# Optimization experiments

Hardware: AMD Instinct MI355X
Metric: run time of the kernel (lower is better)

The kernel has to match this reference:

```python
import jax, jax.numpy as jnp
import numpy as np

B, S, D, M, HID, THETA = 8, 4096, 128, 256, 256, 4096


def _impulse_response():
    """Build discretized LTI (A,B) via ZOH and the impulse response H [M, S]."""
    Q = jnp.arange(M, dtype=jnp.float32).reshape(-1, 1)          # [M,1]
    R = (2.0 * Q + 1.0) / THETA                                   # [M,1]
    ii, jj = jnp.meshgrid(jnp.arange(M), jnp.arange(M), indexing='ij')
    # (-1)^(i-j+1): -1 when (i-j) even, +1 when odd
    sign = jnp.where((ii - jj) % 2 == 0, -1.0, 1.0)
    A = R * jnp.where(ii < jj, -1.0, sign)                        # [M,M]
    Bv = R * jnp.where(jnp.arange(M).reshape(-1, 1) % 2 == 0, 1.0, -1.0)  # [M,1]
    # zero-order-hold discretization via matrix exponential of augmented system
    aug = jnp.zeros((M + 1, M + 1), dtype=jnp.float32)
    aug = aug.at[:M, :M].set(A).at[:M, M].set(Bv[:, 0])
    expA = jax.scipy.linalg.expm(aug)
    Ad, Bd = expA[:M, :M], expA[:M, M:M + 1]
    # H[:, i] = Ad^i @ Bd
    def step(Ai, _):
        return Ad @ Ai, (Ai @ Bd)[:, 0]
    _, Hs = jax.lax.scan(step, jnp.eye(M, dtype=jnp.float32), None, length=S)
    return Hs.T  # [M, S]


def setup_inputs() -> dict:
    key = jax.random.key(0)
    k1, k2, k3 = jax.random.split(key, 3)
    x = jax.random.normal(k1, (B, S, D), dtype=jnp.float32)
    W_u = jax.random.normal(k2, (D, 1), dtype=jnp.float32) / np.sqrt(D)
    b_u = jnp.zeros((1,), dtype=jnp.float32)
    W_h = jax.random.normal(k3, (M + D, HID), dtype=jnp.float32) / np.sqrt(M + D)
    b_h = jnp.zeros((HID,), dtype=jnp.float32)
    H = _impulse_response()  # [M, S], fixed (non-trainable) impulse response
    return {"x": x, "W_u": W_u, "b_u": b_u, "W_h": W_h, "b_h": b_h, "H": H}


def reference(x, W_u, b_u, W_h, b_h, H):
    batch, seq_len, _ = x.shape
    n = 2 * seq_len
    # u_t = relu(W_u x_t)  -> [B, S, 1]
    u = jax.nn.relu(jnp.einsum('bsd,do->bso', x, W_u) + b_u)
    fft_H = jnp.fft.rfft(H, n=n, axis=-1)                 # [M, S+1]
    fft_u = jnp.fft.rfft(u[..., 0], n=n, axis=-1)         # [B, S+1]
    temp = fft_u[:, None, :] * fft_H[None, :, :]          # [B, M, S+1] complex
    m = jnp.fft.irfft(temp, n=n, axis=-1)[:, :, :seq_len]  # [B, M, S]
    m = jnp.transpose(m, (0, 2, 1))                       # [B, S, M]
    input_h = jnp.concatenate([m, x], axis=-1)            # [B, S, M+D]
    h = jax.nn.relu(jnp.einsum('bsf,fh->bsh', input_h, W_h) + b_h)
    h_n = h[:, -1, :]
    return (h, h_n)
```

## Files before the change

### kernel.cpp

```cpp
#include <hip/hip_runtime.h>

#define S_LEN 4096
#define B_SZ 8
#define HN_OFF 8388608
#define CPROWS 544

typedef __attribute__((ext_vector_type(8))) short short8;
typedef __attribute__((ext_vector_type(4))) float f32x4;

typedef const __attribute__((address_space(1))) unsigned int as1_u32;
typedef __attribute__((address_space(3))) unsigned int as3_u32;

__device__ __forceinline__ void gload16(const short* g, short* l) {
  __builtin_amdgcn_global_load_lds((as1_u32*)g, (as3_u32*)l, 16, 0, 0);
}

__device__ __forceinline__ short f2bf(float f) {
  union { float f; unsigned u; } v; v.f = f;
  unsigned r = v.u + 0x7FFFu + ((v.u >> 16) & 1u);
  return (short)(r >> 16);
}

__global__ __launch_bounds__(256) void k_prep(const float* __restrict__ x,
                                              const float* __restrict__ Wu,
                                              const float* __restrict__ bu,
                                              const float* __restrict__ H,
                                              const float* __restrict__ Wh,
                                              short* __restrict__ cp,
                                              short* __restrict__ xb,
                                              short* __restrict__ Ht,
                                              short* __restrict__ wht) {
  int bx = blockIdx.x;
  if (bx >= 8520) {
    int j = (bx - 8520) * 256 + threadIdx.x;
    if (j < 256 * 384) {
      int n = j / 384, k = j % 384;
      wht[j] = f2bf(Wh[k * 256 + n]);
    }
    return;
  }
  if (bx >= 8264) {
    __shared__ short tile[64][72];
    int bx2 = bx - 8264;
    int t0 = (bx2 >> 2) << 6, q0 = (bx2 & 3) << 6;
    int tid = threadIdx.x;
    int r = tid >> 2, c0 = (tid & 3) << 4;
    const float* src = H + (size_t)(q0 + r) * S_LEN + t0 + c0;
    #pragma unroll
    for (int v4 = 0; v4 < 4; ++v4) {
      float4 hv = *(const float4*)(src + 4 * v4);
      tile[r][c0 + 4 * v4]     = f2bf(hv.x);
      tile[r][c0 + 4 * v4 + 1] = f2bf(hv.y);
      tile[r][c0 + 4 * v4 + 2] = f2bf(hv.z);
      tile[r][c0 + 4 * v4 + 3] = f2bf(hv.w);
    }
    __syncthreads();
    int s2 = tid >> 2, qc = (tid & 3) << 4;
    short8 o0, o1;
    #pragma unroll
    for (int j2 = 0; j2 < 8; ++j2) {
      o0[j2] = tile[qc + j2][s2];
      o1[j2] = tile[qc + 8 + j2][s2];
    }
    short* dst = Ht + (size_t)(t0 + s2) * 256 + q0 + qc;
    *(short8*)dst       = o0;
    *(short8*)(dst + 8) = o1;
    return;
  }
  if (bx >= 8192) {
    int idx = (bx - 8192) * 256 + threadIdx.x;
    if (idx < 18432) {
      int j = idx & 7;
      int r = 508 + ((idx >> 3) % 36);
      int rem = (idx >> 3) / 36;
      int p = rem & 7;
      int b = rem >> 3;
      int e = 8 * r + p + j;
      if (e >= S_LEN)
        cp[((size_t)(b * 8 + p) * CPROWS + r) * 8 + j] = 0;
    }
    return;
  }
  int row = bx * 4 + (threadIdx.x >> 6);
  int l = threadIdx.x & 63;
  float2 xv = *(const float2*)(x + (size_t)row * 128 + 2 * l);
  float2 wv = *(const float2*)(Wu + 2 * l);
  float s = xv.x * wv.x + xv.y * wv.y;
  #pragma unroll
  for (int m = 32; m >= 1; m >>= 1) s += __shfl_xor(s, m, 64);
  unsigned pack = (((unsigned)f2bf(xv.y) & 0xFFFFu) << 16) | ((unsigned)f2bf(xv.x) & 0xFFFFu);
  *(unsigned*)(xb + (size_t)row * 128 + 2 * l) = pack;
  float v = s + bu[0];
  v = v > 0.0f ? v : 0.0f;
  short vb = f2bf(v);
  if (l < 8) {
    int t = row & (S_LEN - 1);
    int b = row >> 12;
    int e = (S_LEN - 1) - t;
    int p = l;
    if (e >= p) {
      int d = e - p;
      cp[((size_t)(b * 8 + p) * CPROWS + (d >> 3)) * 8 + (d & 7)] = vb;
    }
  }
}

__global__ __launch_bounds__(256) void k_g(const short* __restrict__ wht,
                                           const short* __restrict__ Ht,
                                           short* __restrict__ Gt) {
  int nt = blockIdx.x & 1, tt = blockIdx.x >> 1;
  int n0 = nt << 7, t0 = tt << 7;
  int tid = threadIdx.x;
  int lane = tid & 63, wid = tid >> 6;
  int wr = wid >> 1, wc = wid & 1;
  int lm = lane & 15, kg = lane >> 4;

  const short* Abase = wht + (size_t)(n0 + wr * 64 + lm) * 384 + 8 * kg;
  const short* Bbase = Ht  + (size_t)(t0 + wc * 64 + lm) * 256 + 8 * kg;

  f32x4 acc[4][4];
  #pragma unroll
  for (int ii = 0; ii < 4; ++ii)
    #pragma unroll
    for (int jn = 0; jn < 4; ++jn)
      acc[ii][jn] = (f32x4){0.0f, 0.0f, 0.0f, 0.0f};

  #pragma unroll
  for (int c = 0; c < 4; ++c) {
    short8 a[8], bf[8];
    #pragma unroll
    for (int mf = 0; mf < 4; ++mf)
      #pragma unroll
      for (int ks = 0; ks < 2; ++ks)
        a[mf * 2 + ks] = *(const short8*)(Abase + mf * 16 * 384 + c * 64 + ks * 32);
    #pragma unroll
    for (int nf = 0; nf < 4; ++nf)
      #pragma unroll
      for (int ks = 0; ks < 2; ++ks)
        bf[nf * 2 + ks] = *(const short8*)(Bbase + nf * 16 * 256 + c * 64 + ks * 32);
    #pragma unroll
    for (int ks = 0; ks < 2; ++ks)
      #pragma unroll
      for (int mf = 0; mf < 4; ++mf)
        #pragma unroll
        for (int nf = 0; nf < 4; ++nf)
          acc[mf][nf] = __builtin_amdgcn_mfma_f32_16x16x32_bf16(a[mf * 2 + ks], bf[nf * 2 + ks], acc[mf][nf], 0, 0, 0);
  }

  #pragma unroll
  for (int mf = 0; mf < 4; ++mf)
    #pragma unroll
    for (int nf = 0; nf < 4; ++nf)
      #pragma unroll
      for (int j = 0; j < 4; ++j) {
        int n = n0 + wr * 64 + mf * 16 + kg * 4 + j;
        int t = t0 + wc * 64 + nf * 16 + lm;
        Gt[(size_t)n * S_LEN + t] = f2bf(acc[mf][nf][j]);
      }
}

__global__ __launch_bounds__(512, 2) void k_fused(const short* __restrict__ cp,
                                                  const short* __restrict__ Gt,
                                                  const short* __restrict__ xb,
                                                  const short* __restrict__ wht,
                                                  const float* __restrict__ bh,
                                                  float* __restrict__ out) {
  __shared__ __attribute__((aligned(16))) short Bt[2][128 * 128];
  __shared__ __attribute__((aligned(16))) short Aw[2][6144];

  int i = blockIdx.x;
  int kk = i >> 4;
  int nt = i & 1;
  int b  = (i >> 1) & 7;
  int n0 = nt << 7;

  int tid = threadIdx.x;
  int lane = tid & 63, wid = tid >> 6;
  int wr = wid >> 2, wc = wid & 3;
  int lm = lane & 15, kg = lane >> 4;
  int l3 = lane >> 3, l7 = lane & 7;
  int lm7 = lm & 7;

  const short* bS0 = Gt + (size_t)(n0 + wid * 16 + kg) * S_LEN + ((lm ^ kg) << 3);
  const short* bS1 = Gt + (size_t)(n0 + wid * 16 + 4 + kg) * S_LEN + ((lm ^ (kg ^ 4)) << 3);

  int dbase = 127 - 64 * wr - lm + 8 * kg;
  int aof[10];
  #pragma unroll
  for (int v = 0; v < 10; ++v) {
    int d = dbase + 16 * v - 48;
    aof[v] = ((d & ~7) | ((d & 7) ^ ((d >> 3) & 7))) << 3;
  }

  int bof[8];
  #pragma unroll
  for (int nf = 0; nf < 2; ++nf)
    #pragma unroll
    for (int ks = 0; ks < 4; ++ks)
      bof[nf * 4 + ks] = (wc * 32 + nf * 16 + lm) * 128 + (((4 * ks + kg) ^ lm7) << 3);

  int xof[16];
  #pragma unroll
  for (int mf = 0; mf < 4; ++mf)
    #pragma unroll
    for (int ks = 0; ks < 4; ++ks)
      xof[mf * 4 + ks] = (wr * 64 + mf * 16 + lm) * 128 + (((4 * ks + kg) ^ lm7) << 3);

  const short* wxBase = wht + (size_t)(n0 + wc * 32 + lm) * 384 + 256 + 8 * kg;

  for (int ph = 0; ph < 2; ++ph) {
    int st = ph ? kk : (31 - kk);
    int s0 = st << 7;
    int asbase = 496 - 16 * st;
    const short* aSrc = cp + ((size_t)(b * 8 + (l7 ^ l3)) * CPROWS + asbase + wid * 8 + l3) * 8;
    const short* xR0 = xb + (size_t)(b * S_LEN + s0 + wid * 16 + kg) * 128 + ((lm ^ kg) << 3);
    const short* xR1 = xb + (size_t)(b * S_LEN + s0 + wid * 16 + 4 + kg) * 128 + ((lm ^ (kg ^ 4)) << 3);

    int NCt = st + 1;
    int NCp = NCt + 1;

    f32x4 acc[4][2];
    #pragma unroll
    for (int ii = 0; ii < 4; ++ii)
      #pragma unroll
      for (int jn = 0; jn < 2; ++jn)
        acc[ii][jn] = (f32x4){0.0f, 0.0f, 0.0f, 0.0f};

    auto STAGE_T = [&](int cc) {
      int slot = cc & 1;
      int coff = cc * 128;
      #pragma unroll
      for (int e = 0; e < 2; ++e) {
        gload16(bS0 + (size_t)(8 * e) * S_LEN + coff, &Bt[slot][(wid * 16 + 8 * e) * 128]);
        gload16(bS1 + (size_t)(8 * e) * S_LEN + coff, &Bt[slot][(wid * 16 + 8 * e + 4) * 128]);
      }
      if (wid < 4) gload16(aSrc + coff, &Aw[slot][wid * 512]);
    };
    auto STAGE_X = [&]() {
      int slot = NCt & 1;
      #pragma unroll
      for (int e = 0; e < 2; ++e) {
        gload16(xR0 + (size_t)(8 * e) * 128, &Bt[slot][(wid * 16 + 8 * e) * 128]);
        gload16(xR1 + (size_t)(8 * e) * 128, &Bt[slot][(wid * 16 + 8 * e + 4) * 128]);
      }
    };

    asm volatile("s_waitcnt vmcnt(0) lgkmcnt(0)\n\ts_barrier" ::: "memory");
    STAGE_T(0);

    for (int c = 0; c < NCp; ++c) {
      asm volatile("s_waitcnt vmcnt(0) lgkmcnt(0)\n\ts_barrier" ::: "memory");
      if (c + 1 < NCt) STAGE_T(c + 1);
      else if (c + 1 < NCp) STAGE_X();

      if (c < NCt) {
        const short* AwB = &Aw[c & 1][0];
        const short* BtB = &Bt[c & 1][0];
        short8 A10[10];
        #pragma unroll
        for (int v = 0; v < 10; ++v) A10[v] = *(const short8*)(AwB + aof[v]);
        short8 Bf[8];
        #pragma unroll
        for (int ii = 0; ii < 8; ++ii) Bf[ii] = *(const short8*)(BtB + bof[ii]);
        __builtin_amdgcn_s_setprio(1);
        #pragma unroll
        for (int ks = 0; ks < 4; ++ks)
          #pragma unroll
          for (int mf = 0; mf < 4; ++mf)
            #pragma unroll
            for (int nf = 0; nf < 2; ++nf)
              acc[mf][nf] = __builtin_amdgcn_mfma_f32_16x16x32_bf16(
                  A10[2 * ks - mf + 3], Bf[nf * 4 + ks], acc[mf][nf], 0, 0, 0);
        __builtin_amdgcn_s_setprio(0);
      } else {
        const short* BtB = &Bt[NCt & 1][0];
        short8 Ax[16];
        #pragma unroll
        for (int ii = 0; ii < 16; ++ii) Ax[ii] = *(const short8*)(BtB + xof[ii]);
        short8 Bx[8];
        #pragma unroll
        for (int nf = 0; nf < 2; ++nf)
          #pragma unroll
          for (int ks = 0; ks < 4; ++ks)
            Bx[nf * 4 + ks] = *(const short8*)(wxBase + (size_t)nf * 16 * 384 + 32 * ks);
        __builtin_amdgcn_s_setprio(1);
        #pragma unroll
        for (int ks = 0; ks < 4; ++ks)
          #pragma unroll
          for (int mf = 0; mf < 4; ++mf)
            #pragma unroll
            for (int nf = 0; nf < 2; ++nf)
              acc[mf][nf] = __builtin_amdgcn_mfma_f32_16x16x32_bf16(
                  Ax[mf * 4 + ks], Bx[nf * 4 + ks], acc[mf][nf], 0, 0, 0);
        __builtin_amdgcn_s_setprio(0);
      }
    }

    #pragma unroll
    for (int mf = 0; mf < 4; ++mf)
      #pragma unroll
      for (int nf = 0; nf < 2; ++nf) {
        int n = n0 + wc * 32 + nf * 16 + lm;
        float bias = bh[n];
        #pragma unroll
        for (int j2 = 0; j2 < 4; ++j2) {
          int s = s0 + wr * 64 + mf * 16 + kg * 4 + j2;
          float v = acc[mf][nf][j2] + bias;
          v = v > 0.0f ? v : 0.0f;
          out[(size_t)(b * S_LEN + s) * 256 + n] = v;
          if (s == S_LEN - 1)
            out[HN_OFF + b * 256 + n] = v;
        }
      }
  }
}

extern "C" void kernel_launch(void* const* d_in, const int* in_sizes, int n_in,
                              void* d_out, int out_size, void* d_ws, size_t ws_size,
                              hipStream_t stream) {
  const float* x  = (const float*)d_in[0];
  const float* Wu = (const float*)d_in[1];
  const float* bu = (const float*)d_in[2];
  const float* Wh = (const float*)d_in[3];
  const float* bh = (const float*)d_in[4];
  const float* H  = (const float*)d_in[5];
  float* out = (float*)d_out;

  char* ws = (char*)d_ws;
  short* cp  = (short*)(ws);
  short* wht = (short*)(ws + 557056);
  short* xb  = (short*)(ws + 753664);
  short* Ht  = (short*)(ws + 9142272);
  short* Gt  = (short*)(ws + 11239424);

  k_prep<<<8904, 256, 0, stream>>>(x, Wu, bu, H, Wh, cp, xb, Ht, wht);
  k_g   <<<64,   256, 0, stream>>>(wht, Ht, Gt);
  k_fused<<<256, 512, 0, stream>>>(cp, Gt, xb, wht, bh, out);
}
```

Measured before the change: 76.34 us.

## Triple-buffer fused Toeplitz GEMM with half-K stages and interleaved loads

Restructures the fused Toeplitz-plus-x GEMM main loop to use 64-wide K chunks with a three-slot LDS ring. Loads are issued two stages ahead and split between the two MFMA half-phases, so global-to-LDS copies overlap with compute. Shared memory per block drops, which lets launch bounds target four blocks per CU instead of two. Block index mapping is also reordered so batch varies fastest. The extra barriers per stage and the higher occupancy target may add sync overhead or register pressure.

```diff
diff --git a/kernel.cpp b/kernel.cpp
--- a/kernel.cpp
+++ b/kernel.cpp
@@ -20,6 +20,8 @@
   unsigned r = v.u + 0x7FFFu + ((v.u >> 16) & 1u);
   return (short)(r >> 16);
 }
+
+#define MFMA(d, a, bb) d = __builtin_amdgcn_mfma_f32_16x16x32_bf16(a, bb, d, 0, 0, 0)
 
 __global__ __launch_bounds__(256) void k_prep(const float* __restrict__ x,
                                               const float* __restrict__ Wu,
@@ -144,7 +146,7 @@
       for (int mf = 0; mf < 4; ++mf)
         #pragma unroll
         for (int nf = 0; nf < 4; ++nf)
-          acc[mf][nf] = __builtin_amdgcn_mfma_f32_16x16x32_bf16(a[mf * 2 + ks], bf[nf * 2 + ks], acc[mf][nf], 0, 0, 0);
+          MFMA(acc[mf][nf], a[mf * 2 + ks], bf[nf * 2 + ks]);
   }
 
   #pragma unroll
@@ -159,65 +161,65 @@
       }
 }
 
-__global__ __launch_bounds__(512, 2) void k_fused(const short* __restrict__ cp,
+__global__ __launch_bounds__(512, 4) void k_fused(const short* __restrict__ cp,
                                                   const short* __restrict__ Gt,
                                                   const short* __restrict__ xb,
                                                   const short* __restrict__ wht,
                                                   const float* __restrict__ bh,
                                                   float* __restrict__ out) {
-  __shared__ __attribute__((aligned(16))) short Bt[2][128 * 128];
-  __shared__ __attribute__((aligned(16))) short Aw[2][6144];
+  __shared__ __attribute__((aligned(16))) short Bt[3][128 * 64];
+  __shared__ __attribute__((aligned(16))) short Aw[3][2048];
 
   int i = blockIdx.x;
   int kk = i >> 4;
-  int nt = i & 1;
-  int b  = (i >> 1) & 7;
+  int nt = (i >> 3) & 1;
+  int b  = i & 7;
   int n0 = nt << 7;
 
   int tid = threadIdx.x;
   int lane = tid & 63, wid = tid >> 6;
   int wr = wid >> 2, wc = wid & 3;
   int lm = lane & 15, kg = lane >> 4;
-  int l3 = lane >> 3, l7 = lane & 7;
+  int l3v = lane >> 3, l7 = lane & 7;
   int lm7 = lm & 7;
 
-  const short* bS0 = Gt + (size_t)(n0 + wid * 16 + kg) * S_LEN + ((lm ^ kg) << 3);
-  const short* bS1 = Gt + (size_t)(n0 + wid * 16 + 4 + kg) * S_LEN + ((lm ^ (kg ^ 4)) << 3);
+  const short* bS0 = Gt + (size_t)(n0 + wid * 8 + l3v) * S_LEN + ((l7 ^ l3v) << 3);
+  const short* bS1 = Gt + (size_t)(n0 + 64 + wid * 8 + l3v) * S_LEN + ((l7 ^ l3v) << 3);
+
+  int la = lane & 31;
+  int G7 = ((wid & 1) << 2) | (la >> 3);
+  int apar = (la & 7) ^ G7;
 
   int dbase = 127 - 64 * wr - lm + 8 * kg;
-  int aof[10];
-  #pragma unroll
-  for (int v = 0; v < 10; ++v) {
-    int d = dbase + 16 * v - 48;
-    aof[v] = ((d & ~7) | ((d & 7) ^ ((d >> 3) & 7))) << 3;
-  }
-
-  int bof[8];
-  #pragma unroll
-  for (int nf = 0; nf < 2; ++nf)
-    #pragma unroll
-    for (int ks = 0; ks < 4; ++ks)
-      bof[nf * 4 + ks] = (wc * 32 + nf * 16 + lm) * 128 + (((4 * ks + kg) ^ lm7) << 3);
-
-  int xof[16];
+  int aof[6];
+  #pragma unroll
+  for (int ii = 0; ii < 6; ++ii) {
+    int d = (ii < 4) ? (dbase - 16 * ii) : (dbase + 96 - 16 * ii);
+    aof[ii] = ((d & ~7) | ((d & 7) ^ ((d >> 3) & 7))) << 3;
+  }
+  int bofk[2][2];
+  #pragma unroll
+  for (int ks = 0; ks < 2; ++ks)
+    #pragma unroll
+    for (int nf = 0; nf < 2; ++nf)
+      bofk[ks][nf] = (wc * 32 + nf * 16 + lm) * 64 + (((ks << 5) + (kg << 3)) ^ (lm7 << 3));
+  int xof[4][2];
   #pragma unroll
   for (int mf = 0; mf < 4; ++mf)
     #pragma unroll
-    for (int ks = 0; ks < 4; ++ks)
-      xof[mf * 4 + ks] = (wr * 64 + mf * 16 + lm) * 128 + (((4 * ks + kg) ^ lm7) << 3);
-
-  const short* wxBase = wht + (size_t)(n0 + wc * 32 + lm) * 384 + 256 + 8 * kg;
+    for (int ks = 0; ks < 2; ++ks)
+      xof[mf][ks] = (wr * 64 + mf * 16 + lm) * 64 + (((ks << 5) + (kg << 3)) ^ (lm7 << 3));
 
   for (int ph = 0; ph < 2; ++ph) {
     int st = ph ? kk : (31 - kk);
     int s0 = st << 7;
     int asbase = 496 - 16 * st;
-    const short* aSrc = cp + ((size_t)(b * 8 + (l7 ^ l3)) * CPROWS + asbase + wid * 8 + l3) * 8;
-    const short* xR0 = xb + (size_t)(b * S_LEN + s0 + wid * 16 + kg) * 128 + ((lm ^ kg) << 3);
-    const short* xR1 = xb + (size_t)(b * S_LEN + s0 + wid * 16 + 4 + kg) * 128 + ((lm ^ (kg ^ 4)) << 3);
-
-    int NCt = st + 1;
-    int NCp = NCt + 1;
+    const short* aSrc = cp + ((size_t)(b * 8 + apar) * CPROWS + asbase + ((wid & 1) ? 4 : 0) + (wid >> 1) * 8 + (la >> 3)) * 8;
+    aSrc = cp + ((size_t)(b * 8 + apar) * CPROWS + asbase + wid * 4 + (la >> 3)) * 8;
+    const short* xH0 = xb + (size_t)(b * S_LEN + s0 + wid * 8 + l3v) * 128 + ((l7 ^ l3v) << 3);
+    const short* xH1 = xb + (size_t)(b * S_LEN + s0 + 64 + wid * 8 + l3v) * 128 + ((l7 ^ l3v) << 3);
+
+    int T = 2 * st + 2;
 
     f32x4 acc[4][2];
     #pragma unroll
@@ -226,74 +228,92 @@
       for (int jn = 0; jn < 2; ++jn)
         acc[ii][jn] = (f32x4){0.0f, 0.0f, 0.0f, 0.0f};
 
-    auto STAGE_T = [&](int cc) {
-      int slot = cc & 1;
-      int coff = cc * 128;
-      #pragma unroll
-      for (int e = 0; e < 2; ++e) {
-        gload16(bS0 + (size_t)(8 * e) * S_LEN + coff, &Bt[slot][(wid * 16 + 8 * e) * 128]);
-        gload16(bS1 + (size_t)(8 * e) * S_LEN + coff, &Bt[slot][(wid * 16 + 8 * e + 4) * 128]);
-      }
-      if (wid < 4) gload16(aSrc + coff, &Aw[slot][wid * 512]);
+    auto STG_B = [&](int cc, int h, int slot) {
+      gload16((h ? bS1 : bS0) + cc * 64, &Bt[slot][h * 4096 + wid * 512]);
     };
-    auto STAGE_X = [&]() {
-      int slot = NCt & 1;
-      #pragma unroll
-      for (int e = 0; e < 2; ++e) {
-        gload16(xR0 + (size_t)(8 * e) * 128, &Bt[slot][(wid * 16 + 8 * e) * 128]);
-        gload16(xR1 + (size_t)(8 * e) * 128, &Bt[slot][(wid * 16 + 8 * e + 4) * 128]);
+    auto STG_A = [&](int cc, int slot) {
+      if (lane < 32) gload16(aSrc + cc * 64, &Aw[slot][wid * 256]);
+      else { asm volatile("" ::: );
       }
     };
-
+    auto STG_X = [&](int xc, int h, int slot) {
+      gload16((h ? xH1 : xH0) + xc * 64, &Bt[slot][h * 4096 + wid * 512]);
+    };
+
+    if (ph) asm volatile("s_waitcnt lgkmcnt(0)\n\ts_barrier" ::: "memory");
+
+    STG_B(0, 0, 0); STG_B(0, 1, 0); STG_A(0, 0);
+    STG_B(1, 0, 1); STG_B(1, 1, 1); STG_A(1, 1);
+
+    int cur = 0;
+    for (int c = 0; c < T; ++c) {
+      if (c + 1 < T) asm volatile("s_waitcnt vmcnt(3)\n\ts_barrier" ::: "memory");
+      else           asm volatile("s_waitcnt vmcnt(0)\n\ts_barrier" ::: "memory");
+      const short* AwB = &Aw[cur][0];
+      const short* BtB = &Bt[cur][0];
+      int tg = (cur >= 1) ? (cur - 1) : 2;
+      short8 A0 = *(const short8*)(AwB + aof[0]);
+      short8 A1 = *(const short8*)(AwB + aof[1]);
+      short8 A2 = *(const short8*)(AwB + aof[2]);
+      short8 A3 = *(const short8*)(AwB + aof[3]);
+      short8 B00 = *(const short8*)(BtB + bofk[0][0]);
+      short8 B01 = *(const short8*)(BtB + bofk[0][1]);
+      if (c + 2 < T) { STG_B(c + 2, 0, tg); STG_A(c + 2, tg); }
+      asm volatile("s_barrier" ::: "memory");
+      __builtin_amdgcn_s_setprio(1);
+      MFMA(acc[0][0], A0, B00); MFMA(acc[0][1], A0, B01);
+      MFMA(acc[1][0], A1, B00); MFMA(acc[1][1], A1, B01);
+      MFMA(acc[2][0], A2, B00); MFMA(acc[2][1], A2, B01);
+      MFMA(acc[3][0], A3, B00); MFMA(acc[3][1], A3, B01);
+      __builtin_amdgcn_s_setprio(0);
+      asm volatile("s_barrier" ::: "memory");
+      short8 A4 = *(const short8*)(AwB + aof[4]);
+      short8 A5 = *(const short8*)(AwB + aof[5]);
+      short8 B10 = *(const short8*)(BtB + bofk[1][0]);
+      short8 B11 = *(const short8*)(BtB + bofk[1][1]);
+      if (c + 2 < T) STG_B(c + 2, 1, tg);
+      asm volatile("s_barrier" ::: "memory");
+      __builtin_amdgcn_s_setprio(1);
+      MFMA(acc[0][0], A4, B10); MFMA(acc[0][1], A4, B11);
+      MFMA(acc[1][0], A5, B10); MFMA(acc[1][1], A5, B11);
+      MFMA(acc[2][0], A0, B10); MFMA(acc[2][1], A0, B11);
+      MFMA(acc[3][0], A1, B10); MFMA(acc[3][1], A1, B11);
+      __builtin_amdgcn_s_setprio(0);
+      asm volatile("s_barrier" ::: "memory");
+      cur = (cur == 2) ? 0 : cur + 1;
+    }
+
+    int sx0 = cur;
+    int sx1 = (cur == 2) ? 0 : cur + 1;
+    STG_X(0, 0, sx0); STG_X(0, 1, sx0);
+    STG_X(1, 0, sx1); STG_X(1, 1, sx1);
+    short8 Bx[2][2][2];
+    #pragma unroll
+    for (int xc = 0; xc < 2; ++xc)
+      #pragma unroll
+      for (int ks = 0; ks < 2; ++ks)
+        #pragma unroll
+        for (int nf = 0; nf < 2; ++nf)
+          Bx[xc][ks][nf] = *(const short8*)(wht + (size_t)(n0 + wc * 32 + nf * 16 + lm) * 384 + 256 + xc * 64 + ks * 32 + kg * 8);
     asm volatile("s_waitcnt vmcnt(0) lgkmcnt(0)\n\ts_barrier" ::: "memory");
-    STAGE_T(0);
-
-    for (int c = 0; c < NCp; ++c) {
-      asm volatile("s_waitcnt vmcnt(0) lgkmcnt(0)\n\ts_barrier" ::: "memory");
-      if (c + 1 < NCt) STAGE_T(c + 1);
-      else if (c + 1 < NCp) STAGE_X();
-
-      if (c < NCt) {
-        const short* AwB = &Aw[c & 1][0];
-        const short* BtB = &Bt[c & 1][0];
-        short8 A10[10];
-        #pragma unroll
-        for (int v = 0; v < 10; ++v) A10[v] = *(const short8*)(AwB + aof[v]);
-        short8 Bf[8];
-        #pragma unroll
-        for (int ii = 0; ii < 8; ++ii) Bf[ii] = *(const short8*)(BtB + bof[ii]);
-        __builtin_amdgcn_s_setprio(1);
-        #pragma unroll
-        for (int ks = 0; ks < 4; ++ks)
+    #pragma unroll
+    for (int xc = 0; xc < 2; ++xc) {
+      const short* XB = &Bt[xc ? sx1 : sx0][0];
+      short8 Ax[4][2];
+      #pragma unroll
+      for (int mf = 0; mf < 4; ++mf)
+        #pragma unroll
+        for (int ks = 0; ks < 2; ++ks)
+          Ax[mf][ks] = *(const short8*)(XB + xof[mf][ks]);
+      __builtin_amdgcn_s_setprio(1);
+      #pragma unroll
+      for (int ks = 0; ks < 2; ++ks)
+        #pragma unroll
+        for (int mf = 0; mf < 4; ++mf)
           #pragma unroll
-          for (int mf = 0; mf < 4; ++mf)
-            #pragma unroll
-            for (int nf = 0; nf < 2; ++nf)
-              acc[mf][nf] = __builtin_amdgcn_mfma_f32_16x16x32_bf16(
-                  A10[2 * ks - mf + 3], Bf[nf * 4 + ks], acc[mf][nf], 0, 0, 0);
-        __builtin_amdgcn_s_setprio(0);
-      } else {
-        const short* BtB = &Bt[NCt & 1][0];
-        short8 Ax[16];
-        #pragma unroll
-        for (int ii = 0; ii < 16; ++ii) Ax[ii] = *(const short8*)(BtB + xof[ii]);
-        short8 Bx[8];
-        #pragma unroll
-        for (int nf = 0; nf < 2; ++nf)
-          #pragma unroll
-          for (int ks = 0; ks < 4; ++ks)
-            Bx[nf * 4 + ks] = *(const short8*)(wxBase + (size_t)nf * 16 * 384 + 32 * ks);
-        __builtin_amdgcn_s_setprio(1);
-        #pragma unroll
-        for (int ks = 0; ks < 4; ++ks)
-          #pragma unroll
-          for (int mf = 0; mf < 4; ++mf)
-            #pragma unroll
-            for (int nf = 0; nf < 2; ++nf)
-              acc[mf][nf] = __builtin_amdgcn_mfma_f32_16x16x32_bf16(
-                  Ax[mf * 4 + ks], Bx[nf * 4 + ks], acc[mf][nf], 0, 0, 0);
-        __builtin_amdgcn_s_setprio(0);
-      }
+          for (int nf = 0; nf < 2; ++nf)
+            MFMA(acc[mf][nf], Ax[mf][ks], Bx[xc][ks][nf]);
+      __builtin_amdgcn_s_setprio(0);
     }
 
     #pragma unroll
```

New measurement: 86.66 us. 1.14x slower.

## Split fused GEMM into 64-column tiles with 4-slot, 2-ahead async pipeline

Applied to the files above, without the earlier changes.

The fused Toeplitz+x GEMM kernel now uses 256-thread blocks that each own 64 output columns instead of 128, doubling the grid to 512 blocks. Staging moves from double buffering with a full drain each step to a 4-slot ring that prefetches two chunks ahead, using partial vmcnt waits so global-to-LDS loads overlap MFMA work. The x-projection tail is split into two 64-wide K chunks that are staged through the same ring. The aim is better occupancy and less load latency exposed per iteration, at the cost of each block re-reading the shared A operand for fewer columns and relying on exact vmcnt counting.

```diff
diff --git a/kernel.cpp b/kernel.cpp
--- a/kernel.cpp
+++ b/kernel.cpp
@@ -20,6 +20,8 @@
   unsigned r = v.u + 0x7FFFu + ((v.u >> 16) & 1u);
   return (short)(r >> 16);
 }
+
+#define MFMA(d, a, bb) d = __builtin_amdgcn_mfma_f32_16x16x32_bf16(a, bb, d, 0, 0, 0)
 
 __global__ __launch_bounds__(256) void k_prep(const float* __restrict__ x,
                                               const float* __restrict__ Wu,
@@ -144,7 +146,7 @@
       for (int mf = 0; mf < 4; ++mf)
         #pragma unroll
         for (int nf = 0; nf < 4; ++nf)
-          acc[mf][nf] = __builtin_amdgcn_mfma_f32_16x16x32_bf16(a[mf * 2 + ks], bf[nf * 2 + ks], acc[mf][nf], 0, 0, 0);
+          MFMA(acc[mf][nf], a[mf * 2 + ks], bf[nf * 2 + ks]);
   }
 
   #pragma unroll
@@ -159,30 +161,30 @@
       }
 }
 
-__global__ __launch_bounds__(512, 2) void k_fused(const short* __restrict__ cp,
+__global__ __launch_bounds__(256, 2) void k_fused(const short* __restrict__ cp,
                                                   const short* __restrict__ Gt,
                                                   const short* __restrict__ xb,
                                                   const short* __restrict__ wht,
                                                   const float* __restrict__ bh,
                                                   float* __restrict__ out) {
-  __shared__ __attribute__((aligned(16))) short Bt[2][128 * 128];
-  __shared__ __attribute__((aligned(16))) short Aw[2][6144];
+  __shared__ __attribute__((aligned(16))) short Bt[4][64 * 128];
+  __shared__ __attribute__((aligned(16))) short Aw[4][2048];
 
   int i = blockIdx.x;
-  int kk = i >> 4;
-  int nt = i & 1;
-  int b  = (i >> 1) & 7;
-  int n0 = nt << 7;
+  int kk = i >> 5;
+  int nq = (i >> 3) & 3;
+  int b  = i & 7;
+  int n0 = nq << 6;
 
   int tid = threadIdx.x;
   int lane = tid & 63, wid = tid >> 6;
-  int wr = wid >> 2, wc = wid & 3;
+  int wr = wid >> 1, wc = wid & 1;
   int lm = lane & 15, kg = lane >> 4;
   int l3 = lane >> 3, l7 = lane & 7;
   int lm7 = lm & 7;
 
   const short* bS0 = Gt + (size_t)(n0 + wid * 16 + kg) * S_LEN + ((lm ^ kg) << 3);
-  const short* bS1 = Gt + (size_t)(n0 + wid * 16 + 4 + kg) * S_LEN + ((lm ^ (kg ^ 4)) << 3);
+  const short* bS1 = Gt + (size_t)(n0 + wid * 16 + 4 + kg) * S_LEN + ((lm ^ (kg | 4)) << 3);
 
   int dbase = 127 - 64 * wr - lm + 8 * kg;
   int aof[10];
@@ -199,25 +201,22 @@
     for (int ks = 0; ks < 4; ++ks)
       bof[nf * 4 + ks] = (wc * 32 + nf * 16 + lm) * 128 + (((4 * ks + kg) ^ lm7) << 3);
 
-  int xof[16];
+  int xof[4][2];
   #pragma unroll
   for (int mf = 0; mf < 4; ++mf)
     #pragma unroll
-    for (int ks = 0; ks < 4; ++ks)
-      xof[mf * 4 + ks] = (wr * 64 + mf * 16 + lm) * 128 + (((4 * ks + kg) ^ lm7) << 3);
-
-  const short* wxBase = wht + (size_t)(n0 + wc * 32 + lm) * 384 + 256 + 8 * kg;
+    for (int ks = 0; ks < 2; ++ks)
+      xof[mf][ks] = (wr * 64 + mf * 16 + lm) * 64 + (((4 * ks + kg) ^ lm7) << 3);
 
   for (int ph = 0; ph < 2; ++ph) {
     int st = ph ? kk : (31 - kk);
     int s0 = st << 7;
     int asbase = 496 - 16 * st;
     const short* aSrc = cp + ((size_t)(b * 8 + (l7 ^ l3)) * CPROWS + asbase + wid * 8 + l3) * 8;
-    const short* xR0 = xb + (size_t)(b * S_LEN + s0 + wid * 16 + kg) * 128 + ((lm ^ kg) << 3);
-    const short* xR1 = xb + (size_t)(b * S_LEN + s0 + wid * 16 + 4 + kg) * 128 + ((lm ^ (kg ^ 4)) << 3);
-
-    int NCt = st + 1;
-    int NCp = NCt + 1;
+    const short* xS = xb + (size_t)(b * S_LEN + s0 + wid * 32 + l3) * 128 + ((l7 ^ l3) << 3);
+
+    int NT = st + 1;
+    int NC = NT + 2;
 
     f32x4 acc[4][2];
     #pragma unroll
@@ -226,36 +225,41 @@
       for (int jn = 0; jn < 2; ++jn)
         acc[ii][jn] = (f32x4){0.0f, 0.0f, 0.0f, 0.0f};
 
-    auto STAGE_T = [&](int cc) {
-      int slot = cc & 1;
-      int coff = cc * 128;
-      #pragma unroll
-      for (int e = 0; e < 2; ++e) {
-        gload16(bS0 + (size_t)(8 * e) * S_LEN + coff, &Bt[slot][(wid * 16 + 8 * e) * 128]);
-        gload16(bS1 + (size_t)(8 * e) * S_LEN + coff, &Bt[slot][(wid * 16 + 8 * e + 4) * 128]);
-      }
-      if (wid < 4) gload16(aSrc + coff, &Aw[slot][wid * 512]);
+    auto STAGE = [&](int cc) {
+      int slot = cc & 3;
+      if (cc < NT) {
+        int coff = cc * 128;
+        gload16(bS0 + coff,                      &Bt[slot][(wid * 16) * 128]);
+        gload16(bS1 + coff,                      &Bt[slot][(wid * 16 + 4) * 128]);
+        gload16(bS0 + (size_t)8 * S_LEN + coff,  &Bt[slot][(wid * 16 + 8) * 128]);
+        gload16(bS1 + (size_t)8 * S_LEN + coff,  &Bt[slot][(wid * 16 + 12) * 128]);
+        gload16(aSrc + coff,                     &Aw[slot][wid * 512]);
+      } else {
+        int dc = cc - NT;
+        #pragma unroll
+        for (int jj = 0; jj < 4; ++jj)
+          gload16(xS + (size_t)(8 * jj) * 128 + dc * 64, &Bt[slot][(wid * 32 + 8 * jj) * 64]);
+        gload16(aSrc, &Aw[slot][wid * 512]);
+      }
     };
-    auto STAGE_X = [&]() {
-      int slot = NCt & 1;
-      #pragma unroll
-      for (int e = 0; e < 2; ++e) {
-        gload16(xR0 + (size_t)(8 * e) * 128, &Bt[slot][(wid * 16 + 8 * e) * 128]);
-        gload16(xR1 + (size_t)(8 * e) * 128, &Bt[slot][(wid * 16 + 8 * e + 4) * 128]);
-      }
-    };
-
-    asm volatile("s_waitcnt vmcnt(0) lgkmcnt(0)\n\ts_barrier" ::: "memory");
-    STAGE_T(0);
-
-    for (int c = 0; c < NCp; ++c) {
-      asm volatile("s_waitcnt vmcnt(0) lgkmcnt(0)\n\ts_barrier" ::: "memory");
-      if (c + 1 < NCt) STAGE_T(c + 1);
-      else if (c + 1 < NCp) STAGE_X();
-
-      if (c < NCt) {
-        const short* AwB = &Aw[c & 1][0];
-        const short* BtB = &Bt[c & 1][0];
+
+    if (ph) asm volatile("s_waitcnt vmcnt(0) lgkmcnt(0)\n\ts_barrier" ::: "memory");
+    STAGE(0);
+    STAGE(1);
+
+    for (int c = 0; c < NC; ++c) {
+      if (c + 2 < NC) {
+        STAGE(c + 2);
+        asm volatile("s_waitcnt vmcnt(10) lgkmcnt(0)\n\ts_barrier" ::: "memory");
+      } else if (c + 1 < NC) {
+        asm volatile("s_waitcnt vmcnt(5) lgkmcnt(0)\n\ts_barrier" ::: "memory");
+      } else {
+        asm volatile("s_waitcnt vmcnt(0) lgkmcnt(0)\n\ts_barrier" ::: "memory");
+      }
+
+      if (c < NT) {
+        const short* AwB = &Aw[c & 3][0];
+        const short* BtB = &Bt[c & 3][0];
         short8 A10[10];
         #pragma unroll
         for (int v = 0; v < 10; ++v) A10[v] = *(const short8*)(AwB + aof[v]);
@@ -269,29 +273,32 @@
           for (int mf = 0; mf < 4; ++mf)
             #pragma unroll
             for (int nf = 0; nf < 2; ++nf)
-              acc[mf][nf] = __builtin_amdgcn_mfma_f32_16x16x32_bf16(
-                  A10[2 * ks - mf + 3], Bf[nf * 4 + ks], acc[mf][nf], 0, 0, 0);
+              MFMA(acc[mf][nf], A10[2 * ks - mf + 3], Bf[nf * 4 + ks]);
         __builtin_amdgcn_s_setprio(0);
       } else {
-        const short* BtB = &Bt[NCt & 1][0];
-        short8 Ax[16];
-        #pragma unroll
-        for (int ii = 0; ii < 16; ++ii) Ax[ii] = *(const short8*)(BtB + xof[ii]);
-        short8 Bx[8];
-        #pragma unroll
-        for (int nf = 0; nf < 2; ++nf)
+        int dc = c - NT;
+        const short* BtB = &Bt[c & 3][0];
+        short8 Ax[4][2];
+        #pragma unroll
+        for (int mf = 0; mf < 4; ++mf)
           #pragma unroll
-          for (int ks = 0; ks < 4; ++ks)
-            Bx[nf * 4 + ks] = *(const short8*)(wxBase + (size_t)nf * 16 * 384 + 32 * ks);
+          for (int ks = 0; ks < 2; ++ks)
+            Ax[mf][ks] = *(const short8*)(BtB + xof[mf][ks]);
+        short8 Bx[2][2];
+        #pragma unroll
+        for (int ks = 0; ks < 2; ++ks)
+          #pragma unroll
+          for (int nf = 0; nf < 2; ++nf)
+            Bx[ks][nf] = *(const short8*)(wht + (size_t)(n0 + wc * 32 + nf * 16 + lm) * 384
+                                          + 256 + dc * 64 + ks * 32 + kg * 8);
         __builtin_amdgcn_s_setprio(1);
         #pragma unroll
-        for (int ks = 0; ks < 4; ++ks)
+        for (int ks = 0; ks < 2; ++ks)
           #pragma unroll
           for (int mf = 0; mf < 4; ++mf)
             #pragma unroll
             for (int nf = 0; nf < 2; ++nf)
-              acc[mf][nf] = __builtin_amdgcn_mfma_f32_16x16x32_bf16(
-                  Ax[mf * 4 + ks], Bx[nf * 4 + ks], acc[mf][nf], 0, 0, 0);
+              MFMA(acc[mf][nf], Ax[mf][ks], Bx[ks][nf]);
         __builtin_amdgcn_s_setprio(0);
       }
     }
@@ -335,5 +342,5 @@
 
   k_prep<<<8904, 256, 0, stream>>>(x, Wu, bu, H, Wh, cp, xb, Ht, wht);
   k_g   <<<64,   256, 0, stream>>>(wht, Ht, Gt);
-  k_fused<<<256, 512, 0, stream>>>(cp, Gt, xb, wht, bh, out);
-}
+  k_fused<<<512, 256, 0, stream>>>(cp, Gt, xb, wht, bh, out);
+}
```

Result: faster. 67.12 us (-12.1%).
